# Kernel optimization log

Hardware: AMD Instinct MI355X
Metric: run time of the kernel (lower is better)

The kernel has to match this reference:

```python
import jax, jax.numpy as jnp
import numpy as np

D = 300      # d_model / entity_embed_size, hard-coded in the module
TOPK = 20    # k in torch.topk


def setup_inputs() -> dict:
    key = jax.random.key(0)
    ks = jax.random.split(key, 6)
    N, T = 2, 4096
    scale = 1.0 / np.sqrt(D).astype(np.float32)
    return {
        "querys": jax.random.normal(ks[0], (N, T, D), jnp.float32),
        "keys":   jax.random.normal(ks[1], (N, T, D), jnp.float32),
        "values": jax.random.normal(ks[2], (N, T, D), jnp.float32),
        "Wq": jax.random.normal(ks[3], (D, D), jnp.float32) * scale,
        "Wk": jax.random.normal(ks[4], (D, D), jnp.float32) * scale,
        "Wv": jax.random.normal(ks[5], (D, D), jnp.float32) * scale,
        "num_heads": 6,
    }


def reference(querys, keys, values, Wq, Wk, Wv, num_heads):
    N, Tq, d = querys.shape
    h = int(num_heads)
    dh = d // h  # head dim (must divide; 300/6 = 50)

    # nn.Linear(bias=False): y = x @ W^T
    Q = querys @ Wq.T
    K = keys @ Wk.T
    V = values @ Wv.T  # computed but unused by the 'selected' attention, kept for fidelity

    # torch.cat(torch.split(X, dh, dim=2), dim=0): head index becomes major batch dim
    def to_heads(X):
        n, t, _ = X.shape
        return X.reshape(n, t, h, dh).transpose(2, 0, 1, 3).reshape(h * n, t, dh)

    Q_, K_ = to_heads(Q), to_heads(K)

    # scaled_dot_selected_product_attention
    scores = jnp.einsum('bqd,bkd->bqk', Q_, K_) / (dh ** 0.5)  # [hN, Tq, Tk]
    max_att = scores.max(axis=1)                                # [hN, Tk] (max over queries)
    top_vals, top_ids = jax.lax.top_k(max_att, TOPK)            # [hN, 20]
    probs = jax.nn.softmax(top_vals, axis=-1)                   # [hN, 20]
    # gather from K (not V!), matching the original code
    sel = jnp.take_along_axis(K_, top_ids[:, :, None], axis=1)  # [hN, 20, dh]
    out = jnp.sum(sel * probs[:, :, None], axis=1, keepdims=True)  # [hN, 1, dh]

    # torch.cat(torch.split(outputs, N, dim=0), dim=2): merge heads back on feature dim
    out = out.reshape(h, N, 1, dh).transpose(1, 2, 0, 3).reshape(N, 1, d)
    return out
```

## Files before the change

kernel.cpp:

```cpp
#include <hip/hip_runtime.h>
#include <hip/hip_bf16.h>
#include <math.h>

#define T      4096
#define Dm     300
#define NH     6
#define DH     50
#define NB     2
#define NBATCH 12
#define KTOP   20
#define NCAND  48
#define QC     8
#define RQC    16
#define NBINS  4096
#define BMAX   1024
#define WCH    30720

typedef short  bs8  __attribute__((ext_vector_type(8)));
typedef float  f4   __attribute__((ext_vector_type(4)));

static __device__ __forceinline__ unsigned short f2bf(float f) {
    union { float f; unsigned u; } x{f};
    unsigned r = x.u + 0x7fffu + ((x.u >> 16) & 1u);
    return (unsigned short)(r >> 16);
}
static __device__ __forceinline__ float bf2f(unsigned short h) {
    union { unsigned u; float f; } x;
    x.u = ((unsigned)h) << 16;
    return x.f;
}
static __device__ __forceinline__ unsigned fkey(float f) {
    unsigned u = __float_as_uint(f);
    return (u & 0x80000000u) ? ~u : (u | 0x80000000u);
}

__global__ __launch_bounds__(256) void wfrag_kernel(
    const float* __restrict__ Wq, const float* __restrict__ Wk,
    unsigned short* __restrict__ Whf, unsigned short* __restrict__ Wlf)
{
    const int idx = blockIdx.x * 256 + threadIdx.x;
    if (idx >= WCH) return;
    const int lane = idx & 63, rest = idx >> 6;
    const int ks = rest % 10, r2 = rest / 10;
    const int nt = r2 & 1, r3 = r2 >> 1;
    const int jtg = r3 % 12, z = r3 / 12;
    const int n16 = lane & 15, quad = lane >> 4;
    const int j = jtg * 32 + nt * 16 + n16;
    const int head = j >> 6, dd = j & 63;
    const float* W = z ? Wk : Wq;

    bs8 vh, vl;
#pragma unroll
    for (int e = 0; e < 8; ++e) {
        int k = ks * 32 + quad * 8 + e;
        float v = (dd < DH && k < 300) ? W[(head * DH + dd) * 300 + (k < 300 ? k : 0)] : 0.f;
        unsigned short h = f2bf(v);
        vh[e] = (short)h;
        vl[e] = (short)f2bf(v - bf2f(h));
    }
    *(bs8*)(Whf + (size_t)idx * 8) = vh;
    *(bs8*)(Wlf + (size_t)idx * 8) = vl;
}

__global__ __launch_bounds__(256, 1) void proj_mfma_kernel(
    const float* __restrict__ Xq, const float* __restrict__ Xk,
    const unsigned short* __restrict__ Whf, const unsigned short* __restrict__ Wlf,
    float* __restrict__ Qt, float* __restrict__ Kt,
    unsigned short* __restrict__ Qb, unsigned short* __restrict__ Kb)
{
    __shared__ unsigned short Bsh[2][2560 * 8];
    __shared__ unsigned short Tr[4][32][40];

    const int z  = blockIdx.z;
    const int jg = blockIdx.y;
    const int m0 = blockIdx.x * 128;
    const float* X = z ? Xk : Xq;
    float*          Ytf = z ? Kt : Qt;
    unsigned short* Ytb = z ? Kb : Qb;

    const int tid = threadIdx.x;
    const int wave = tid >> 6, lane = tid & 63;
    const int m16 = lane & 15, quad = lane >> 4;
    const int n = m0 >> 12, t0 = m0 & (T - 1);

    bs8 Ah[2][10], Al[2][10];
#pragma unroll
    for (int mt = 0; mt < 2; ++mt) {
        const float* rowp = X + (size_t)(m0 + wave * 32 + mt * 16 + m16) * 300;
#pragma unroll
        for (int ks = 0; ks < 10; ++ks) {
            float f[8];
            if (ks < 9) {
                float4 a = *(const float4*)(rowp + ks * 32 + quad * 8);
                float4 c = *(const float4*)(rowp + ks * 32 + quad * 8 + 4);
                f[0] = a.x; f[1] = a.y; f[2] = a.z; f[3] = a.w;
                f[4] = c.x; f[5] = c.y; f[6] = c.z; f[7] = c.w;
            } else {
#pragma unroll
                for (int e = 0; e < 8; ++e) {
                    int k = 288 + quad * 8 + e;
                    f[e] = (k < 300) ? rowp[k < 300 ? k : 0] : 0.f;
                }
            }
#pragma unroll
            for (int e = 0; e < 8; ++e) {
                unsigned short h = f2bf(f[e]);
                Ah[mt][ks][e] = (short)h;
                Al[mt][ks][e] = (short)f2bf(f[e] - bf2f(h));
            }
        }
    }

    bs8 rh[5], rl[5];
    {
        size_t cb = (size_t)(z * 12 + jg * 6) * 1280;
#pragma unroll
        for (int i = 0; i < 5; ++i) {
            int c = i * 256 + tid;
            rh[i] = *(const bs8*)(Whf + (cb + c) * 8);
            rl[i] = *(const bs8*)(Wlf + (cb + c) * 8);
        }
#pragma unroll
        for (int i = 0; i < 5; ++i) {
            int c = i * 256 + tid;
            *(bs8*)&Bsh[0][c * 8]          = rh[i];
            *(bs8*)&Bsh[0][(1280 + c) * 8] = rl[i];
        }
    }

    f4 acc[2][2] = {{{0.f,0.f,0.f,0.f},{0.f,0.f,0.f,0.f}},
                    {{0.f,0.f,0.f,0.f},{0.f,0.f,0.f,0.f}}};

    for (int jt = 0; jt < 6; ++jt) {
        __syncthreads();

        if (jt < 5) {
            size_t cb = (size_t)(z * 12 + jg * 6 + jt + 1) * 1280;
#pragma unroll
            for (int i = 0; i < 5; ++i) {
                int c = i * 256 + tid;
                rh[i] = *(const bs8*)(Whf + (cb + c) * 8);
                rl[i] = *(const bs8*)(Wlf + (cb + c) * 8);
            }
        }

        const unsigned short* Bbuf = Bsh[jt & 1];
#pragma unroll
        for (int ks = 0; ks < 10; ++ks) {
#pragma unroll
            for (int nt = 0; nt < 2; ++nt) {
                bs8 bh = *(const bs8*)&Bbuf[((nt * 10 + ks) * 64 + lane) * 8];
                bs8 bl = *(const bs8*)&Bbuf[((1280 + (nt * 10 + ks) * 64) + lane) * 8];
#pragma unroll
                for (int mt = 0; mt < 2; ++mt) {
                    acc[mt][nt] = __builtin_amdgcn_mfma_f32_16x16x32_bf16(Ah[mt][ks], bh, acc[mt][nt], 0, 0, 0);
                    acc[mt][nt] = __builtin_amdgcn_mfma_f32_16x16x32_bf16(Al[mt][ks], bh, acc[mt][nt], 0, 0, 0);
                    acc[mt][nt] = __builtin_amdgcn_mfma_f32_16x16x32_bf16(Ah[mt][ks], bl, acc[mt][nt], 0, 0, 0);
                }
            }
        }

        const int jtg  = jg * 6 + jt;
        const int head = jtg >> 1, d0 = (jtg & 1) * 32;
        const int b    = head * NB + n;

#pragma unroll
        for (int nt = 0; nt < 2; ++nt) {
            const int dd = d0 + nt * 16 + m16;
            if (dd < DH) {
                float* base = Ytf + ((size_t)b * DH + dd) * T + t0 + wave * 32;
#pragma unroll
                for (int mt = 0; mt < 2; ++mt)
                    *(float4*)(base + mt * 16 + quad * 4) =
                        make_float4(acc[mt][nt][0], acc[mt][nt][1], acc[mt][nt][2], acc[mt][nt][3]);
            }
        }

#pragma unroll
        for (int mt = 0; mt < 2; ++mt)
#pragma unroll
            for (int nt = 0; nt < 2; ++nt)
#pragma unroll
                for (int r = 0; r < 4; ++r)
                    Tr[wave][mt * 16 + quad * 4 + r][nt * 16 + m16] = f2bf(acc[mt][nt][r]);
        {
            const int rr = lane >> 1, p = lane & 1;
            unsigned short* dst = Ytb + ((size_t)b * T + t0 + wave * 32 + rr) * 64 + d0 + p * 16;
            *(bs8*)dst       = *(const bs8*)&Tr[wave][rr][p * 16];
            *(bs8*)(dst + 8) = *(const bs8*)&Tr[wave][rr][p * 16 + 8];
        }

#pragma unroll
        for (int mt = 0; mt < 2; ++mt)
#pragma unroll
            for (int nt = 0; nt < 2; ++nt)
                acc[mt][nt] = (f4){0.f, 0.f, 0.f, 0.f};

        __syncthreads();
        if (jt < 5) {
#pragma unroll
            for (int i = 0; i < 5; ++i) {
                int c = i * 256 + tid;
                *(bs8*)&Bsh[(jt + 1) & 1][c * 8]          = rh[i];
                *(bs8*)&Bsh[(jt + 1) & 1][(1280 + c) * 8] = rl[i];
            }
        }
    }
}

__global__ __launch_bounds__(256) void score_mfma_kernel(
    const unsigned short* __restrict__ Qb, const unsigned short* __restrict__ Kb,
    float* __restrict__ pamax)
{
    __shared__ unsigned short Qlds[1024 * 8];

    const int kb   = blockIdx.x;
    const int b    = blockIdx.y;
    const int qc   = blockIdx.z;
    const int tid  = threadIdx.x;
    const int wave = tid >> 6, lane = tid & 63;
    const int m16  = lane & 15, quad = lane >> 4;

    const int k0 = kb * 256 + wave * 64;

    bs8 Bf[4][2];
#pragma unroll
    for (int kt = 0; kt < 4; ++kt)
#pragma unroll
        for (int h = 0; h < 2; ++h)
            Bf[kt][h] = *(const bs8*)(Kb + ((size_t)(b * T + k0 + kt * 16 + m16)) * 64
                                         + quad * 8 + h * 32);

    float cmax[4];
#pragma unroll
    for (int kt = 0; kt < 4; ++kt) cmax[kt] = -INFINITY;

    for (int it = 0; it < 4; ++it) {
        const int q0 = qc * 512 + it * 128;
        __syncthreads();
#pragma unroll
        for (int i = 0; i < 4; ++i) {
            int idx = i * 256 + tid;
            int r = idx >> 3, c2 = idx & 7;
            int ch = r * 8 + (c2 ^ (r & 7));
            *(bs8*)&Qlds[ch * 8] =
                *(const bs8*)(Qb + ((size_t)(b * T + q0 + r)) * 64 + c2 * 8);
        }
        __syncthreads();

#pragma unroll
        for (int mt = 0; mt < 8; ++mt) {
            const int row = mt * 16 + m16;
            bs8 A0 = *(const bs8*)&Qlds[(row * 8 + (quad ^ (row & 7))) * 8];
            bs8 A1 = *(const bs8*)&Qlds[(row * 8 + ((quad + 4) ^ (row & 7))) * 8];
#pragma unroll
            for (int kt = 0; kt < 4; ++kt) {
                f4 acc = {0.f, 0.f, 0.f, 0.f};
                acc = __builtin_amdgcn_mfma_f32_16x16x32_bf16(A0, Bf[kt][0], acc, 0, 0, 0);
                acc = __builtin_amdgcn_mfma_f32_16x16x32_bf16(A1, Bf[kt][1], acc, 0, 0, 0);
                cmax[kt] = fmaxf(cmax[kt],
                                 fmaxf(fmaxf(acc[0], acc[1]), fmaxf(acc[2], acc[3])));
            }
        }
    }

#pragma unroll
    for (int kt = 0; kt < 4; ++kt) {
        float v = cmax[kt];
        v = fmaxf(v, __shfl_xor(v, 16));
        v = fmaxf(v, __shfl_xor(v, 32));
        cmax[kt] = v;
    }
    if (lane < 16) {
#pragma unroll
        for (int kt = 0; kt < 4; ++kt)
            pamax[((size_t)qc * NBATCH + b) * T + k0 + kt * 16 + lane] = cmax[kt];
    }
}

__global__ __launch_bounds__(256) void cand_kernel(
    const float* __restrict__ pamax, int* __restrict__ cand)
{
    __shared__ float vals[T];
    __shared__ int   hist[NBINS];
    __shared__ int   part[256];
    __shared__ int   bidx[BMAX];
    __shared__ float bval[BMAX];
    __shared__ int   sh_B, sh_c1, sh_nout, sh_nb;

    const int b = blockIdx.x, tid = threadIdx.x;

    for (int i = tid; i < NBINS; i += 256) hist[i] = 0;
    if (tid == 0) { sh_nout = 0; sh_nb = 0; }
    __syncthreads();

    for (int i = tid; i < T; i += 256) {
        float m = pamax[(size_t)b * T + i];
#pragma unroll
        for (int c = 1; c < QC; ++c)
            m = fmaxf(m, pamax[((size_t)c * NBATCH + b) * T + i]);
        vals[i] = m;
        atomicAdd(&hist[fkey(m) >> 20], 1);
    }
    __syncthreads();

    {
        int s = 0;
#pragma unroll
        for (int k = 0; k < 16; ++k) s += hist[tid * 16 + k];
        part[tid] = s;
        __syncthreads();
        for (int off = 1; off < 256; off <<= 1) {
            int v = (tid + off < 256) ? part[tid + off] : 0;
            __syncthreads();
            part[tid] += v;
            __syncthreads();
        }
        int run = (tid < 255) ? part[tid + 1] : 0;
        for (int k = 15; k >= 0; --k) {
            int bin = tid * 16 + k;
            int c = hist[bin];
            if (run < NCAND && run + c >= NCAND) { sh_B = bin; sh_c1 = run; }
            run += c;
        }
    }
    __syncthreads();

    const int B = sh_B;

    for (int i = tid; i < T; i += 256) {
        int kb = (int)(fkey(vals[i]) >> 20);
        if (kb > B) {
            int p = atomicAdd(&sh_nout, 1);
            cand[b * NCAND + p] = i;
        } else if (kb == B) {
            int p = atomicAdd(&sh_nb, 1);
            if (p < BMAX) { bidx[p] = i; bval[p] = vals[i]; }
        }
    }
    __syncthreads();

    const int c1   = sh_nout;
    const int need = NCAND - c1;
    const int nb   = (sh_nb < BMAX) ? sh_nb : BMAX;
    if (tid < 64) {
        for (int l = 0; l < need; ++l) {
            float mv = -INFINITY; int mp = -1, mt = 0x7fffffff;
            for (int j = tid; j < nb; j += 64) {
                float v = bval[j]; int t = bidx[j];
                if (v > mv || (v == mv && t < mt)) { mv = v; mp = j; mt = t; }
            }
#pragma unroll
            for (int off = 32; off > 0; off >>= 1) {
                float v2 = __shfl_xor(mv, off);
                int   p2 = __shfl_xor(mp, off);
                int   t2 = __shfl_xor(mt, off);
                if (v2 > mv || (v2 == mv && t2 < mt)) { mv = v2; mp = p2; mt = t2; }
            }
            if (tid == 0)
                cand[b * NCAND + c1 + l] = (mp >= 0) ? bidx[mp] : l;
            if (mp >= 0 && tid == (mp & 63)) bval[mp] = -INFINITY;
        }
    }
}

__global__ __launch_bounds__(256) void rescore_kernel(
    const float* __restrict__ Qt, const float* __restrict__ Kt,
    const int* __restrict__ cand, float* __restrict__ rmax)
{
    __shared__ float KcT[DH][NCAND];
    __shared__ float red[4][NCAND];

    const int b = blockIdx.x, qch = blockIdx.y;
    const int tid = threadIdx.x;
    const int lane = tid & 63, wv = tid >> 6;

    for (int i = tid; i < NCAND * DH; i += 256) {
        int j = i / DH, d = i - j * DH;
        KcT[d][j] = Kt[((size_t)b * DH + d) * T + cand[b * NCAND + j]];
    }
    __syncthreads();

    const int q = qch * 256 + tid;
    float qv[DH];
#pragma unroll
    for (int d = 0; d < DH; ++d)
        qv[d] = Qt[((size_t)b * DH + d) * T + q];

    for (int g = 0; g < NCAND / 8; ++g) {
        float cm[8];
#pragma unroll
        for (int j = 0; j < 8; ++j) cm[j] = 0.f;
#pragma unroll
        for (int d = 0; d < DH; ++d) {
            float4 ka = *(const float4*)&KcT[d][g * 8];
            float4 kb = *(const float4*)&KcT[d][g * 8 + 4];
            cm[0] = fmaf(qv[d], ka.x, cm[0]);
            cm[1] = fmaf(qv[d], ka.y, cm[1]);
            cm[2] = fmaf(qv[d], ka.z, cm[2]);
            cm[3] = fmaf(qv[d], ka.w, cm[3]);
            cm[4] = fmaf(qv[d], kb.x, cm[4]);
            cm[5] = fmaf(qv[d], kb.y, cm[5]);
            cm[6] = fmaf(qv[d], kb.z, cm[6]);
            cm[7] = fmaf(qv[d], kb.w, cm[7]);
        }
#pragma unroll
        for (int j = 0; j < 8; ++j) {
            float v = cm[j];
#pragma unroll
            for (int off = 32; off > 0; off >>= 1)
                v = fmaxf(v, __shfl_xor(v, off));
            if (lane == 0) red[wv][g * 8 + j] = v;
        }
    }
    __syncthreads();

    if (tid < NCAND) {
        float v = fmaxf(fmaxf(red[0][tid], red[1][tid]),
                        fmaxf(red[2][tid], red[3][tid]));
        rmax[((size_t)qch * NBATCH + b) * NCAND + tid] = v;
    }
}

__global__ __launch_bounds__(64) void final_kernel(
    const float* __restrict__ rmax, const int* __restrict__ cand,
    const float* __restrict__ Kt, float* __restrict__ out)
{
    __shared__ float selval[KTOP];
    __shared__ int   selidx[KTOP];
    __shared__ float probs[KTOP];

    const int b = blockIdx.x;
    const int lane = threadIdx.x;

    float v = -INFINITY; int idx = 0x7fffffff;
    if (lane < NCAND) {
        v = rmax[(size_t)b * NCAND + lane];
#pragma unroll
        for (int c = 1; c < RQC; ++c)
            v = fmaxf(v, rmax[((size_t)c * NBATCH + b) * NCAND + lane]);
        v *= 0.14142135623730951f;
        idx = cand[b * NCAND + lane];
    }

    for (int l = 0; l < KTOP; ++l) {
        float mv = v; int mi = idx;
#pragma unroll
        for (int off = 32; off > 0; off >>= 1) {
            float v2 = __shfl_xor(mv, off);
            int   i2 = __shfl_xor(mi, off);
            if (v2 > mv || (v2 == mv && i2 < mi)) { mv = v2; mi = i2; }
        }
        if (idx == mi) v = -INFINITY;
        if (lane == 0) { selval[l] = mv; selidx[l] = mi; }
    }
    __syncthreads();

    if (lane == 0) {
        float m = selval[0];
        float s = 0.f;
        for (int l = 0; l < KTOP; ++l) { float e = expf(selval[l] - m); probs[l] = e; s += e; }
        float inv = 1.f / s;
        for (int l = 0; l < KTOP; ++l) probs[l] *= inv;
    }
    __syncthreads();

    if (lane < DH) {
        float acc = 0.f;
#pragma unroll
        for (int l = 0; l < KTOP; ++l)
            acc += probs[l] * Kt[((size_t)b * DH + lane) * T + selidx[l]];
        int head = b / NB, n = b % NB;
        out[n * Dm + head * DH + lane] = acc;
    }
}

extern "C" void kernel_launch(void* const* d_in, const int* in_sizes, int n_in,
                              void* d_out, int out_size, void* d_ws, size_t ws_size,
                              hipStream_t stream) {
    const float* querys = (const float*)d_in[0];
    const float* keys   = (const float*)d_in[1];
    const float* Wq     = (const float*)d_in[3];
    const float* Wk     = (const float*)d_in[4];

    float* out = (float*)d_out;
    float* ws  = (float*)d_ws;

    float* Qt    = ws;
    float* Kt    = Qt + (size_t)NBATCH * DH * T;
    float* pamax = Kt + (size_t)NBATCH * DH * T;
    float* rmax  = pamax + (size_t)QC * NBATCH * T;
    unsigned short* Qb = (unsigned short*)(rmax + (size_t)RQC * NBATCH * NCAND + 8);
    Qb = (unsigned short*)(((uintptr_t)Qb + 15) & ~(uintptr_t)15);
    unsigned short* Kb  = Qb  + (size_t)NBATCH * T * 64;
    unsigned short* Whf = Kb  + (size_t)NBATCH * T * 64;
    unsigned short* Wlf = Whf + (size_t)WCH * 8;
    int* cand = (int*)(Wlf + (size_t)WCH * 8);

    wfrag_kernel    <<<(WCH + 255) / 256, 256, 0, stream>>>(Wq, Wk, Whf, Wlf);
    proj_mfma_kernel<<<dim3(64, 2, 2), 256, 0, stream>>>(querys, keys, Whf, Wlf, Qt, Kt, Qb, Kb);
    score_mfma_kernel<<<dim3(16, NBATCH, QC), 256, 0, stream>>>(Qb, Kb, pamax);
    cand_kernel     <<<NBATCH, 256, 0, stream>>>(pamax, cand);
    rescore_kernel  <<<dim3(NBATCH, RQC), 256, 0, stream>>>(Qt, Kt, cand, rmax);
    final_kernel    <<<NBATCH, 64, 0, stream>>>(rmax, cand, Kt, out);
}
```

Measured before the change: 215.1 us.

## Fuse candidate, rescore and final kernels; atomicMax partial maxes; double-buffer Q tiles

The score kernel now writes per-key maxima with atomicMax on order-preserving unsigned keys into one buffer, instead of writing QC partial arrays. QC drops from 8 to 4, and Q tiles are double-buffered in LDS with register prefetch. The candidate selection, rescoring and final top-k/softmax kernels are merged into one kernel. Each of the RQC blocks recomputes the candidate set, and the last block to finish (tracked by an atomic done counter) does the final reduction. This removes two launches and the partial-max traffic, at the cost of redundant candidate selection in every block, atomics, and init zeroing folded into wfrag_kernel.

```diff
diff --git a/kernel.cpp b/kernel.cpp
--- a/kernel.cpp
+++ b/kernel.cpp
@@ -10,11 +10,12 @@
 #define NBATCH 12
 #define KTOP   20
 #define NCAND  48
-#define QC     8
+#define QC     4
 #define RQC    16
 #define NBINS  4096
 #define BMAX   1024
 #define WCH    30720
+#define INITN  (NBATCH * T + NBATCH * NCAND + NBATCH)
 
 typedef short  bs8  __attribute__((ext_vector_type(8)));
 typedef float  f4   __attribute__((ext_vector_type(4)));
@@ -33,11 +34,19 @@
     unsigned u = __float_as_uint(f);
     return (u & 0x80000000u) ? ~u : (u | 0x80000000u);
 }
+static __device__ __forceinline__ float fkey_inv(unsigned u) {
+    return (u & 0x80000000u) ? __uint_as_float(u & 0x7fffffffu)
+                             : __uint_as_float(~u);
+}
 
 __global__ __launch_bounds__(256) void wfrag_kernel(
     const float* __restrict__ Wq, const float* __restrict__ Wk,
-    unsigned short* __restrict__ Whf, unsigned short* __restrict__ Wlf)
+    unsigned short* __restrict__ Whf, unsigned short* __restrict__ Wlf,
+    unsigned* __restrict__ initp)
 {
+    for (unsigned g = blockIdx.x * 256 + threadIdx.x; g < INITN; g += gridDim.x * 256)
+        initp[g] = 0u;
+
     const int idx = blockIdx.x * 256 + threadIdx.x;
     if (idx >= WCH) return;
     const int lane = idx & 63, rest = idx >> 6;
@@ -210,9 +219,9 @@
 
 __global__ __launch_bounds__(256) void score_mfma_kernel(
     const unsigned short* __restrict__ Qb, const unsigned short* __restrict__ Kb,
-    float* __restrict__ pamax)
+    unsigned* __restrict__ pamax1)
 {
-    __shared__ unsigned short Qlds[1024 * 8];
+    __shared__ unsigned short Qlds[2][1024 * 8];
 
     const int kb   = blockIdx.x;
     const int b    = blockIdx.y;
@@ -235,24 +244,32 @@
 #pragma unroll
     for (int kt = 0; kt < 4; ++kt) cmax[kt] = -INFINITY;
 
-    for (int it = 0; it < 4; ++it) {
-        const int q0 = qc * 512 + it * 128;
+    const int r_ = tid >> 3, c2_ = tid & 7;
+    bs8 pre[4];
+#pragma unroll
+    for (int i = 0; i < 4; ++i)
+        pre[i] = *(const bs8*)(Qb + ((size_t)(b * T + qc * 1024 + i * 32 + r_)) * 64 + c2_ * 8);
+#pragma unroll
+    for (int i = 0; i < 4; ++i) {
+        int row = i * 32 + r_;
+        *(bs8*)&Qlds[0][(row * 8 + (c2_ ^ (row & 7))) * 8] = pre[i];
+    }
+
+    for (int it = 0; it < 8; ++it) {
         __syncthreads();
-#pragma unroll
-        for (int i = 0; i < 4; ++i) {
-            int idx = i * 256 + tid;
-            int r = idx >> 3, c2 = idx & 7;
-            int ch = r * 8 + (c2 ^ (r & 7));
-            *(bs8*)&Qlds[ch * 8] =
-                *(const bs8*)(Qb + ((size_t)(b * T + q0 + r)) * 64 + c2 * 8);
-        }
-        __syncthreads();
-
+        if (it < 7) {
+            const int q0 = qc * 1024 + (it + 1) * 128;
+#pragma unroll
+            for (int i = 0; i < 4; ++i)
+                pre[i] = *(const bs8*)(Qb + ((size_t)(b * T + q0 + i * 32 + r_)) * 64 + c2_ * 8);
+        }
+
+        const unsigned short* Ql = Qlds[it & 1];
 #pragma unroll
         for (int mt = 0; mt < 8; ++mt) {
             const int row = mt * 16 + m16;
-            bs8 A0 = *(const bs8*)&Qlds[(row * 8 + (quad ^ (row & 7))) * 8];
-            bs8 A1 = *(const bs8*)&Qlds[(row * 8 + ((quad + 4) ^ (row & 7))) * 8];
+            bs8 A0 = *(const bs8*)&Ql[(row * 8 + (quad ^ (row & 7))) * 8];
+            bs8 A1 = *(const bs8*)&Ql[(row * 8 + ((quad + 4) ^ (row & 7))) * 8];
 #pragma unroll
             for (int kt = 0; kt < 4; ++kt) {
                 f4 acc = {0.f, 0.f, 0.f, 0.f};
@@ -262,6 +279,14 @@
                                  fmaxf(fmaxf(acc[0], acc[1]), fmaxf(acc[2], acc[3])));
             }
         }
+        __syncthreads();
+        if (it < 7) {
+#pragma unroll
+            for (int i = 0; i < 4; ++i) {
+                int row = i * 32 + r_;
+                *(bs8*)&Qlds[(it + 1) & 1][(row * 8 + (c2_ ^ (row & 7))) * 8] = pre[i];
+            }
+        }
     }
 
 #pragma unroll
@@ -269,41 +294,44 @@
         float v = cmax[kt];
         v = fmaxf(v, __shfl_xor(v, 16));
         v = fmaxf(v, __shfl_xor(v, 32));
-        cmax[kt] = v;
-    }
-    if (lane < 16) {
-#pragma unroll
-        for (int kt = 0; kt < 4; ++kt)
-            pamax[((size_t)qc * NBATCH + b) * T + k0 + kt * 16 + lane] = cmax[kt];
-    }
-}
-
-__global__ __launch_bounds__(256) void cand_kernel(
-    const float* __restrict__ pamax, int* __restrict__ cand)
+        if (lane < 16)
+            atomicMax(&pamax1[(size_t)b * T + k0 + kt * 16 + lane], fkey(v));
+    }
+}
+
+__global__ __launch_bounds__(256) void candrescore_kernel(
+    const unsigned* __restrict__ pamax1,
+    const float* __restrict__ Qt, const float* __restrict__ Kt,
+    unsigned* __restrict__ rmax1, unsigned* __restrict__ done_ct,
+    float* __restrict__ out)
 {
-    __shared__ float vals[T];
-    __shared__ int   hist[NBINS];
-    __shared__ int   part[256];
-    __shared__ int   bidx[BMAX];
-    __shared__ float bval[BMAX];
-    __shared__ int   sh_B, sh_c1, sh_nout, sh_nb;
-
-    const int b = blockIdx.x, tid = threadIdx.x;
+    __shared__ unsigned vals[T];
+    __shared__ int      hist[NBINS];
+    __shared__ int      part[256];
+    __shared__ int      bidx[BMAX];
+    __shared__ unsigned bval[BMAX];
+    __shared__ int      candtmp[NCAND];
+    __shared__ int      cand_s[NCAND];
+    __shared__ float    KcT[DH][NCAND];
+    __shared__ float    red[4][NCAND];
+    __shared__ int      sh_B, sh_nout, sh_nb, sh_pos;
+    __shared__ float    selval[KTOP];
+    __shared__ int      selidx[KTOP];
+    __shared__ float    probs[KTOP];
+
+    const int b = blockIdx.x, qch = blockIdx.y;
+    const int tid = threadIdx.x, lane = tid & 63, wv = tid >> 6;
 
     for (int i = tid; i < NBINS; i += 256) hist[i] = 0;
     if (tid == 0) { sh_nout = 0; sh_nb = 0; }
     __syncthreads();
 
     for (int i = tid; i < T; i += 256) {
-        float m = pamax[(size_t)b * T + i];
-#pragma unroll
-        for (int c = 1; c < QC; ++c)
-            m = fmaxf(m, pamax[((size_t)c * NBATCH + b) * T + i]);
-        vals[i] = m;
-        atomicAdd(&hist[fkey(m) >> 20], 1);
-    }
-    __syncthreads();
-
+        unsigned k = pamax1[(size_t)b * T + i];
+        vals[i] = k;
+        atomicAdd(&hist[k >> 20], 1);
+    }
+    __syncthreads();
     {
         int s = 0;
 #pragma unroll
@@ -320,64 +348,56 @@
         for (int k = 15; k >= 0; --k) {
             int bin = tid * 16 + k;
             int c = hist[bin];
-            if (run < NCAND && run + c >= NCAND) { sh_B = bin; sh_c1 = run; }
+            if (run < NCAND && run + c >= NCAND) sh_B = bin;
             run += c;
         }
     }
     __syncthreads();
-
     const int B = sh_B;
 
     for (int i = tid; i < T; i += 256) {
-        int kb = (int)(fkey(vals[i]) >> 20);
-        if (kb > B) {
+        int kb2 = (int)(vals[i] >> 20);
+        if (kb2 > B) {
             int p = atomicAdd(&sh_nout, 1);
-            cand[b * NCAND + p] = i;
-        } else if (kb == B) {
+            candtmp[p] = i;
+        } else if (kb2 == B) {
             int p = atomicAdd(&sh_nb, 1);
             if (p < BMAX) { bidx[p] = i; bval[p] = vals[i]; }
         }
     }
     __syncthreads();
-
-    const int c1   = sh_nout;
-    const int need = NCAND - c1;
-    const int nb   = (sh_nb < BMAX) ? sh_nb : BMAX;
+    const int c1 = sh_nout, need = NCAND - c1;
+    const int nb = (sh_nb < BMAX) ? sh_nb : BMAX;
     if (tid < 64) {
         for (int l = 0; l < need; ++l) {
-            float mv = -INFINITY; int mp = -1, mt = 0x7fffffff;
+            unsigned mv = 0; int mp = -1, mt = 0x7fffffff;
             for (int j = tid; j < nb; j += 64) {
-                float v = bval[j]; int t = bidx[j];
+                unsigned v = bval[j]; int t = bidx[j];
                 if (v > mv || (v == mv && t < mt)) { mv = v; mp = j; mt = t; }
             }
 #pragma unroll
             for (int off = 32; off > 0; off >>= 1) {
-                float v2 = __shfl_xor(mv, off);
-                int   p2 = __shfl_xor(mp, off);
-                int   t2 = __shfl_xor(mt, off);
+                unsigned v2 = (unsigned)__shfl_xor((int)mv, off);
+                int p2 = __shfl_xor(mp, off);
+                int t2 = __shfl_xor(mt, off);
                 if (v2 > mv || (v2 == mv && t2 < mt)) { mv = v2; mp = p2; mt = t2; }
             }
-            if (tid == 0)
-                cand[b * NCAND + c1 + l] = (mp >= 0) ? bidx[mp] : l;
-            if (mp >= 0 && tid == (mp & 63)) bval[mp] = -INFINITY;
-        }
-    }
-}
-
-__global__ __launch_bounds__(256) void rescore_kernel(
-    const float* __restrict__ Qt, const float* __restrict__ Kt,
-    const int* __restrict__ cand, float* __restrict__ rmax)
-{
-    __shared__ float KcT[DH][NCAND];
-    __shared__ float red[4][NCAND];
-
-    const int b = blockIdx.x, qch = blockIdx.y;
-    const int tid = threadIdx.x;
-    const int lane = tid & 63, wv = tid >> 6;
+            if (tid == 0) candtmp[c1 + l] = (mp >= 0) ? bidx[mp] : 0;
+            if (mp >= 0 && tid == (mp & 63)) bval[mp] = 0;
+        }
+    }
+    __syncthreads();
+
+    if (tid < NCAND) {
+        int myt = candtmp[tid], rank = 0;
+        for (int j = 0; j < NCAND; ++j) rank += (candtmp[j] < myt);
+        cand_s[rank] = myt;
+    }
+    __syncthreads();
 
     for (int i = tid; i < NCAND * DH; i += 256) {
         int j = i / DH, d = i - j * DH;
-        KcT[d][j] = Kt[((size_t)b * DH + d) * T + cand[b * NCAND + j]];
+        KcT[d][j] = Kt[((size_t)b * DH + d) * T + cand_s[j]];
     }
     __syncthreads();
 
@@ -394,15 +414,15 @@
 #pragma unroll
         for (int d = 0; d < DH; ++d) {
             float4 ka = *(const float4*)&KcT[d][g * 8];
-            float4 kb = *(const float4*)&KcT[d][g * 8 + 4];
+            float4 kb2 = *(const float4*)&KcT[d][g * 8 + 4];
             cm[0] = fmaf(qv[d], ka.x, cm[0]);
             cm[1] = fmaf(qv[d], ka.y, cm[1]);
             cm[2] = fmaf(qv[d], ka.z, cm[2]);
             cm[3] = fmaf(qv[d], ka.w, cm[3]);
-            cm[4] = fmaf(qv[d], kb.x, cm[4]);
-            cm[5] = fmaf(qv[d], kb.y, cm[5]);
-            cm[6] = fmaf(qv[d], kb.z, cm[6]);
-            cm[7] = fmaf(qv[d], kb.w, cm[7]);
+            cm[4] = fmaf(qv[d], kb2.x, cm[4]);
+            cm[5] = fmaf(qv[d], kb2.y, cm[5]);
+            cm[6] = fmaf(qv[d], kb2.z, cm[6]);
+            cm[7] = fmaf(qv[d], kb2.w, cm[7]);
         }
 #pragma unroll
         for (int j = 0; j < 8; ++j) {
@@ -414,49 +434,40 @@
         }
     }
     __syncthreads();
-
     if (tid < NCAND) {
         float v = fmaxf(fmaxf(red[0][tid], red[1][tid]),
                         fmaxf(red[2][tid], red[3][tid]));
-        rmax[((size_t)qch * NBATCH + b) * NCAND + tid] = v;
-    }
-}
-
-__global__ __launch_bounds__(64) void final_kernel(
-    const float* __restrict__ rmax, const int* __restrict__ cand,
-    const float* __restrict__ Kt, float* __restrict__ out)
-{
-    __shared__ float selval[KTOP];
-    __shared__ int   selidx[KTOP];
-    __shared__ float probs[KTOP];
-
-    const int b = blockIdx.x;
-    const int lane = threadIdx.x;
-
-    float v = -INFINITY; int idx = 0x7fffffff;
-    if (lane < NCAND) {
-        v = rmax[(size_t)b * NCAND + lane];
-#pragma unroll
-        for (int c = 1; c < RQC; ++c)
-            v = fmaxf(v, rmax[((size_t)c * NBATCH + b) * NCAND + lane]);
-        v *= 0.14142135623730951f;
-        idx = cand[b * NCAND + lane];
-    }
-
-    for (int l = 0; l < KTOP; ++l) {
-        float mv = v; int mi = idx;
-#pragma unroll
-        for (int off = 32; off > 0; off >>= 1) {
-            float v2 = __shfl_xor(mv, off);
-            int   i2 = __shfl_xor(mi, off);
-            if (v2 > mv || (v2 == mv && i2 < mi)) { mv = v2; mi = i2; }
-        }
-        if (idx == mi) v = -INFINITY;
-        if (lane == 0) { selval[l] = mv; selidx[l] = mi; }
-    }
-    __syncthreads();
-
-    if (lane == 0) {
+        atomicMax(&rmax1[b * NCAND + tid], fkey(v));
+    }
+    __syncthreads();
+    if (tid == 0) {
+        __threadfence();
+        sh_pos = atomicAdd(&done_ct[b], 1u);
+    }
+    __syncthreads();
+    if (sh_pos != RQC - 1) return;
+
+    if (tid < 64) {
+        float v = -INFINITY; int idx = 0x7fffffff;
+        if (lane < NCAND) {
+            unsigned u = atomicMax(&rmax1[b * NCAND + lane], 0u);
+            v = fkey_inv(u) * 0.14142135623730951f;
+            idx = cand_s[lane];
+        }
+        for (int l = 0; l < KTOP; ++l) {
+            float mv = v; int mi = idx;
+#pragma unroll
+            for (int off = 32; off > 0; off >>= 1) {
+                float v2 = __shfl_xor(mv, off);
+                int   i2 = __shfl_xor(mi, off);
+                if (v2 > mv || (v2 == mv && i2 < mi)) { mv = v2; mi = i2; }
+            }
+            if (idx == mi) v = -INFINITY;
+            if (lane == 0) { selval[l] = mv; selidx[l] = mi; }
+        }
+    }
+    __syncthreads();
+    if (tid == 0) {
         float m = selval[0];
         float s = 0.f;
         for (int l = 0; l < KTOP; ++l) { float e = expf(selval[l] - m); probs[l] = e; s += e; }
@@ -464,14 +475,13 @@
         for (int l = 0; l < KTOP; ++l) probs[l] *= inv;
     }
     __syncthreads();
-
-    if (lane < DH) {
+    if (tid < DH) {
         float acc = 0.f;
 #pragma unroll
         for (int l = 0; l < KTOP; ++l)
-            acc += probs[l] * Kt[((size_t)b * DH + lane) * T + selidx[l]];
+            acc += probs[l] * Kt[((size_t)b * DH + tid) * T + selidx[l]];
         int head = b / NB, n = b % NB;
-        out[n * Dm + head * DH + lane] = acc;
+        out[n * Dm + head * DH + tid] = acc;
     }
 }
 
@@ -486,21 +496,19 @@
     float* out = (float*)d_out;
     float* ws  = (float*)d_ws;
 
-    float* Qt    = ws;
-    float* Kt    = Qt + (size_t)NBATCH * DH * T;
-    float* pamax = Kt + (size_t)NBATCH * DH * T;
-    float* rmax  = pamax + (size_t)QC * NBATCH * T;
-    unsigned short* Qb = (unsigned short*)(rmax + (size_t)RQC * NBATCH * NCAND + 8);
+    float* Qt = ws;
+    float* Kt = Qt + (size_t)NBATCH * DH * T;
+    unsigned* pamax1  = (unsigned*)(Kt + (size_t)NBATCH * DH * T);
+    unsigned* rmax1   = pamax1 + (size_t)NBATCH * T;
+    unsigned* done_ct = rmax1 + (size_t)NBATCH * NCAND;
+    unsigned short* Qb = (unsigned short*)(done_ct + NBATCH + 4);
     Qb = (unsigned short*)(((uintptr_t)Qb + 15) & ~(uintptr_t)15);
     unsigned short* Kb  = Qb  + (size_t)NBATCH * T * 64;
     unsigned short* Whf = Kb  + (size_t)NBATCH * T * 64;
     unsigned short* Wlf = Whf + (size_t)WCH * 8;
-    int* cand = (int*)(Wlf + (size_t)WCH * 8);
-
-    wfrag_kernel    <<<(WCH + 255) / 256, 256, 0, stream>>>(Wq, Wk, Whf, Wlf);
-    proj_mfma_kernel<<<dim3(64, 2, 2), 256, 0, stream>>>(querys, keys, Whf, Wlf, Qt, Kt, Qb, Kb);
-    score_mfma_kernel<<<dim3(16, NBATCH, QC), 256, 0, stream>>>(Qb, Kb, pamax);
-    cand_kernel     <<<NBATCH, 256, 0, stream>>>(pamax, cand);
-    rescore_kernel  <<<dim3(NBATCH, RQC), 256, 0, stream>>>(Qt, Kt, cand, rmax);
-    final_kernel    <<<NBATCH, 64, 0, stream>>>(rmax, cand, Kt, out);
-}
+
+    wfrag_kernel     <<<(WCH + 255) / 256, 256, 0, stream>>>(Wq, Wk, Whf, Wlf, pamax1);
+    proj_mfma_kernel <<<dim3(64, 2, 2), 256, 0, stream>>>(querys, keys, Whf, Wlf, Qt, Kt, Qb, Kb);
+    score_mfma_kernel<<<dim3(16, NBATCH, QC), 256, 0, stream>>>(Qb, Kb, pamax1);
+    candrescore_kernel<<<dim3(NBATCH, RQC), 256, 0, stream>>>(pamax1, Qt, Kt, rmax1, done_ct, out);
+}
```

New measurement: 205.3 us. 4.5% less time.
